# Kernel optimization log

Measured on AMD Instinct MI355X. Metric: run time of the kernel, lower is better.

Reference implementation:

```python
import jax, jax.numpy as jnp
import numpy as np

N, IN_DIM, OUT_DIM = 8192, 512, 256


def setup_inputs() -> dict:
    key = jax.random.key(0)
    k1, k2, k3, k4 = jax.random.split(key, 4)
    x = jax.random.normal(k1, (N, IN_DIM), dtype=jnp.float32)
    adj = jax.random.randint(k2, (N, N), 0, 2, dtype=jnp.int32)
    # nn.Linear(in_dim, out_dim, bias=False).weight -> [out_dim, in_dim]
    W_proj = jax.random.normal(k3, (OUT_DIM, IN_DIM), dtype=jnp.float32) * (1.0 / np.sqrt(IN_DIM))
    # nn.Linear(2*out_dim, 1, bias=False).weight flattened -> [2*out_dim]
    a = jax.random.normal(k4, (2 * OUT_DIM,), dtype=jnp.float32) * (1.0 / np.sqrt(2 * OUT_DIM))
    return {"x": x, "adj": adj, "W_proj": W_proj, "a": a}


def reference(x, adj, W_proj, a):
    # h = proj(x): [N, D]
    h = x @ W_proj.T
    D = h.shape[-1]
    # attn(cat([h_i, h_j])) == h_i @ a[:D] + h_j @ a[D:]  (exact decomposition,
    # avoids materializing the [N, N, 2D] concat tensor)
    s_i = h @ a[:D]   # [N]
    s_j = h @ a[D:]   # [N]
    scores = s_i[:, None] + s_j[None, :]          # [N, N]
    scores = jnp.where(adj > 0, scores, -jnp.inf)  # masked_fill
    alpha = jax.nn.softmax(scores, axis=1)         # softmax over neighbors j
    # dropout is identity in eval mode
    out = alpha @ h                                # [N, D]
    return jax.nn.elu(out), alpha
```

## Files before the change

kernel.cpp:

```cpp
#include <hip/hip_runtime.h>
#include <hip/hip_bf16.h>

#define NR 8192
#define DIN 512
#define DD 256

typedef __attribute__((ext_vector_type(8))) short short8;
typedef __attribute__((ext_vector_type(4))) float f32x4;

static __device__ __forceinline__ unsigned short f2bf(float x) {
    __hip_bfloat16 b = __float2bfloat16(x);
    return __builtin_bit_cast(unsigned short, b);
}
static __device__ __forceinline__ float bf2f(unsigned short u) {
    unsigned v = ((unsigned)u) << 16;
    return __builtin_bit_cast(float, v);
}

__global__ __launch_bounds__(256) void k_gemm_h(
        const float* __restrict__ x, const float* __restrict__ W,
        float* __restrict__ h) {
    __shared__ unsigned short Ah[64][72], Al[64][72];
    __shared__ unsigned short Bh[128][72], Bl[128][72];
    const int t = threadIdx.x;
    const int i0 = blockIdx.x * 64;
    const int n0 = blockIdx.y * 128;
    const int lane = t & 63, q = lane >> 4, lm = lane & 15;
    const int w = t >> 6, wm = w >> 1, wn = w & 1;
    const int ar = t >> 2, ac0 = (t & 3) << 4;
    const int bn = t >> 1, bh0 = (t & 1) << 5;
    f32x4 acc[2][4];
#pragma unroll
    for (int mt = 0; mt < 2; ++mt)
#pragma unroll
        for (int nt = 0; nt < 4; ++nt) acc[mt][nt] = (f32x4){0.f, 0.f, 0.f, 0.f};

    for (int kb = 0; kb < DIN; kb += 64) {
        __syncthreads();
        {
            const float4* xp = (const float4*)(x + (size_t)(i0 + ar) * DIN + kb + ac0);
#pragma unroll
            for (int u = 0; u < 4; ++u) {
                float4 v = xp[u];
                unsigned short h0 = f2bf(v.x), h1 = f2bf(v.y), h2 = f2bf(v.z), h3 = f2bf(v.w);
                unsigned short l0 = f2bf(v.x - bf2f(h0)), l1 = f2bf(v.y - bf2f(h1));
                unsigned short l2 = f2bf(v.z - bf2f(h2)), l3 = f2bf(v.w - bf2f(h3));
                *(uint2*)&Ah[ar][ac0 + u * 4] =
                    make_uint2((unsigned)h0 | ((unsigned)h1 << 16), (unsigned)h2 | ((unsigned)h3 << 16));
                *(uint2*)&Al[ar][ac0 + u * 4] =
                    make_uint2((unsigned)l0 | ((unsigned)l1 << 16), (unsigned)l2 | ((unsigned)l3 << 16));
            }
            const float4* wp = (const float4*)(W + (size_t)(n0 + bn) * DIN + kb + bh0);
#pragma unroll
            for (int u = 0; u < 8; ++u) {
                float4 v = wp[u];
                unsigned short h0 = f2bf(v.x), h1 = f2bf(v.y), h2 = f2bf(v.z), h3 = f2bf(v.w);
                unsigned short l0 = f2bf(v.x - bf2f(h0)), l1 = f2bf(v.y - bf2f(h1));
                unsigned short l2 = f2bf(v.z - bf2f(h2)), l3 = f2bf(v.w - bf2f(h3));
                *(uint2*)&Bh[bn][bh0 + u * 4] =
                    make_uint2((unsigned)h0 | ((unsigned)h1 << 16), (unsigned)h2 | ((unsigned)h3 << 16));
                *(uint2*)&Bl[bn][bh0 + u * 4] =
                    make_uint2((unsigned)l0 | ((unsigned)l1 << 16), (unsigned)l2 | ((unsigned)l3 << 16));
            }
        }
        __syncthreads();
#pragma unroll
        for (int ks = 0; ks < 64; ks += 32) {
            short8 fa_h[2], fa_l[2], fb_h[4], fb_l[4];
#pragma unroll
            for (int mt = 0; mt < 2; ++mt) {
                int r = wm * 32 + mt * 16 + lm;
                fa_h[mt] = *(const short8*)&Ah[r][ks + q * 8];
                fa_l[mt] = *(const short8*)&Al[r][ks + q * 8];
            }
#pragma unroll
            for (int nt = 0; nt < 4; ++nt) {
                int c = wn * 64 + nt * 16 + lm;
                fb_h[nt] = *(const short8*)&Bh[c][ks + q * 8];
                fb_l[nt] = *(const short8*)&Bl[c][ks + q * 8];
            }
#pragma unroll
            for (int mt = 0; mt < 2; ++mt)
#pragma unroll
                for (int nt = 0; nt < 4; ++nt) {
                    acc[mt][nt] = __builtin_amdgcn_mfma_f32_16x16x32_bf16(fa_h[mt], fb_h[nt], acc[mt][nt], 0, 0, 0);
                    acc[mt][nt] = __builtin_amdgcn_mfma_f32_16x16x32_bf16(fa_h[mt], fb_l[nt], acc[mt][nt], 0, 0, 0);
                    acc[mt][nt] = __builtin_amdgcn_mfma_f32_16x16x32_bf16(fa_l[mt], fb_h[nt], acc[mt][nt], 0, 0, 0);
                }
        }
    }
#pragma unroll
    for (int mt = 0; mt < 2; ++mt)
#pragma unroll
        for (int nt = 0; nt < 4; ++nt)
#pragma unroll
            for (int rr = 0; rr < 4; ++rr) {
                int row = i0 + wm * 32 + mt * 16 + q * 4 + rr;
                int col = n0 + wn * 64 + nt * 16 + lm;
                h[(size_t)row * DD + col] = acc[mt][nt][rr];
            }
}

__global__ __launch_bounds__(256) void k_s(
        const float* __restrict__ h, const float* __restrict__ a,
        float* __restrict__ s, float* __restrict__ pmax) {
    __shared__ float wmax[4];
    const int t = threadIdx.x, w = t >> 6, lane = t & 63;
    const int row = blockIdx.x * 4 + w;
    float4 hv = *(const float4*)(h + (size_t)row * DD + lane * 4);
    float4 av = *(const float4*)(a + DD + lane * 4);
    float d = hv.x * av.x + hv.y * av.y + hv.z * av.z + hv.w * av.w;
#pragma unroll
    for (int off = 32; off; off >>= 1) d += __shfl_down(d, off);
    if (lane == 0) { s[row] = d; wmax[w] = d; }
    __syncthreads();
    if (t == 0)
        pmax[blockIdx.x] = fmaxf(fmaxf(wmax[0], wmax[1]), fmaxf(wmax[2], wmax[3]));
}

__global__ __launch_bounds__(1024) void k_e(
        const float* __restrict__ s, const float* __restrict__ pmax,
        float* __restrict__ e) {
    __shared__ float red[1024];
    const int t = threadIdx.x;
    red[t] = fmaxf(pmax[t], pmax[t + 1024]);
    __syncthreads();
    for (int off = 512; off; off >>= 1) {
        if (t < off) red[t] = fmaxf(red[t], red[t + off]);
        __syncthreads();
    }
    float M = red[0];
    for (int j = t; j < NR; j += 1024) e[j] = expf(s[j] - M);
}

__global__ __launch_bounds__(256) void k_gt(
        const float* __restrict__ h, const float* __restrict__ e,
        unsigned short* __restrict__ gt) {
    __shared__ float tile[64][68];
    const int t = threadIdx.x;
    const int j0 = blockIdx.x * 64, d0 = blockIdx.y * 64;
    const int r = t >> 4, c4 = (t & 15) * 4;
#pragma unroll
    for (int rr = 0; rr < 4; ++rr) {
        int row = r + rr * 16;
        *(float4*)&tile[row][c4] = *(const float4*)(h + (size_t)(j0 + row) * DD + d0 + c4);
    }
    __syncthreads();
    float4 ev = *(const float4*)(e + j0 + c4);
#pragma unroll
    for (int rr = 0; rr < 4; ++rr) {
        int dd = r + rr * 16;
        unsigned short o0 = f2bf(ev.x * tile[c4 + 0][dd]);
        unsigned short o1 = f2bf(ev.y * tile[c4 + 1][dd]);
        unsigned short o2 = f2bf(ev.z * tile[c4 + 2][dd]);
        unsigned short o3 = f2bf(ev.w * tile[c4 + 3][dd]);
        *(uint2*)(gt + (size_t)(d0 + dd) * NR + j0 + c4) =
            make_uint2((unsigned)o0 | ((unsigned)o1 << 16), (unsigned)o2 | ((unsigned)o3 << 16));
    }
}

__global__ __launch_bounds__(512) void k_big(
        const int* __restrict__ adj, const unsigned short* __restrict__ gt,
        const float* __restrict__ e, float* __restrict__ num,
        float* __restrict__ dnm) {
    __shared__ unsigned short As[128][72];
    __shared__ unsigned short Bs[256][72];
    const int t = threadIdx.x;
    const int row0 = blockIdx.x * 128;
    const int k0 = blockIdx.y * 2048;
    const int lane = t & 63, q = lane >> 4, lm = lane & 15;
    const int w = t >> 6, wm = w >> 2, wn = w & 3;
    const int ar = t >> 2, ac0 = (t & 3) << 4;
    const int bn = t >> 1, bh0 = (t & 1) << 5;
    f32x4 acc[4][4];
#pragma unroll
    for (int mt = 0; mt < 4; ++mt)
#pragma unroll
        for (int nt = 0; nt < 4; ++nt) acc[mt][nt] = (f32x4){0.f, 0.f, 0.f, 0.f};
    float dsum = 0.f;

    for (int it = 0; it < 32; ++it) {
        const int kb = k0 + it * 64;
        __syncthreads();
        {
            const int4* ap = (const int4*)(adj + (size_t)(row0 + ar) * NR + kb + ac0);
            const float4* ep = (const float4*)(e + kb + ac0);
#pragma unroll
            for (int u = 0; u < 4; ++u) {
                int4 av = ap[u];
                float4 ev = ep[u];
                unsigned p0 = (av.x ? 0x3F80u : 0u) | (av.y ? 0x3F800000u : 0u);
                unsigned p1 = (av.z ? 0x3F80u : 0u) | (av.w ? 0x3F800000u : 0u);
                dsum += (av.x ? ev.x : 0.f) + (av.y ? ev.y : 0.f) +
                        (av.z ? ev.z : 0.f) + (av.w ? ev.w : 0.f);
                *(uint2*)&As[ar][ac0 + u * 4] = make_uint2(p0, p1);
            }
            const int4* gp = (const int4*)(gt + (size_t)bn * NR + kb + bh0);
            int4* bd = (int4*)&Bs[bn][bh0];
#pragma unroll
            for (int u = 0; u < 4; ++u) bd[u] = gp[u];
        }
        __syncthreads();
#pragma unroll
        for (int ks = 0; ks < 64; ks += 32) {
            short8 fa[4], fb[4];
#pragma unroll
            for (int mt = 0; mt < 4; ++mt)
                fa[mt] = *(const short8*)&As[wm * 64 + mt * 16 + lm][ks + q * 8];
#pragma unroll
            for (int nt = 0; nt < 4; ++nt)
                fb[nt] = *(const short8*)&Bs[wn * 64 + nt * 16 + lm][ks + q * 8];
#pragma unroll
            for (int mt = 0; mt < 4; ++mt)
#pragma unroll
                for (int nt = 0; nt < 4; ++nt)
                    acc[mt][nt] = __builtin_amdgcn_mfma_f32_16x16x32_bf16(fa[mt], fb[nt], acc[mt][nt], 0, 0, 0);
        }
    }
    dsum += __shfl_xor(dsum, 1);
    dsum += __shfl_xor(dsum, 2);
    if ((t & 3) == 0) atomicAdd(&dnm[row0 + ar], dsum);
#pragma unroll
    for (int mt = 0; mt < 4; ++mt)
#pragma unroll
        for (int nt = 0; nt < 4; ++nt)
#pragma unroll
            for (int rr = 0; rr < 4; ++rr) {
                int i = row0 + wm * 64 + mt * 16 + q * 4 + rr;
                int d = wn * 64 + nt * 16 + lm;
                atomicAdd(&num[(size_t)i * DD + d], acc[mt][nt][rr]);
            }
}

__global__ __launch_bounds__(256) void k_fin(
        const float* __restrict__ num, const float* __restrict__ dnm,
        float* __restrict__ out0, float* __restrict__ invd) {
    const int idx = blockIdx.x * 256 + threadIdx.x;
    const int i = idx >> 6, d4 = (idx & 63) << 2;
    float inv = 1.0f / dnm[i];
    float4 nm = *(const float4*)(num + (size_t)i * DD + d4);
    float4 o;
    float z;
    z = nm.x * inv; o.x = z > 0.f ? z : expm1f(z);
    z = nm.y * inv; o.y = z > 0.f ? z : expm1f(z);
    z = nm.z * inv; o.z = z > 0.f ? z : expm1f(z);
    z = nm.w * inv; o.w = z > 0.f ? z : expm1f(z);
    *(float4*)(out0 + (size_t)i * DD + d4) = o;
    if (d4 == 0) invd[i] = inv;
}

__global__ __launch_bounds__(256) void k_alpha(
        const int* __restrict__ adj, const float* __restrict__ e,
        const float* __restrict__ invd, float* __restrict__ alpha) {
    const size_t idx = (size_t)blockIdx.x * 256 + threadIdx.x;
    const int i = (int)(idx >> 11);
    const int jg = (int)(idx & 2047);
    int4 av = ((const int4*)adj)[idx];
    float4 ev = ((const float4*)e)[jg];
    float inv = invd[i];
    float4 o;
    o.x = av.x ? ev.x * inv : 0.f;
    o.y = av.y ? ev.y * inv : 0.f;
    o.z = av.z ? ev.z * inv : 0.f;
    o.w = av.w ? ev.w * inv : 0.f;
    ((float4*)alpha)[idx] = o;
}

extern "C" void kernel_launch(void* const* d_in, const int* in_sizes, int n_in,
                              void* d_out, int out_size, void* d_ws, size_t ws_size,
                              hipStream_t stream) {
    const float* x = (const float*)d_in[0];
    const int* adj = (const int*)d_in[1];
    const float* W = (const float*)d_in[2];
    const float* a = (const float*)d_in[3];
    float* out0 = (float*)d_out;
    float* alpha = (float*)d_out + (size_t)NR * DD;

    char* ws = (char*)d_ws;
    float* h            = (float*)(ws + 0);
    float* s            = (float*)(ws + 8388608);
    float* pmax         = (float*)(ws + 8421376);
    float* e            = (float*)(ws + 8429568);
    float* invd         = (float*)(ws + 8462336);
    float* dnm          = (float*)(ws + 8495104);
    unsigned short* gt  = (unsigned short*)(ws + 8527872);
    float* num          = (float*)(ws + 12722176);

    hipMemsetAsync(num, 0, (size_t)NR * DD * sizeof(float), stream);
    hipMemsetAsync(dnm, 0, NR * sizeof(float), stream);

    k_gemm_h<<<dim3(128, 2), 256, 0, stream>>>(x, W, h);
    k_s<<<2048, 256, 0, stream>>>(h, a, s, pmax);
    k_e<<<1, 1024, 0, stream>>>(s, pmax, e);
    k_gt<<<dim3(128, 4), 256, 0, stream>>>(h, e, gt);
    k_big<<<dim3(64, 4), 512, 0, stream>>>(adj, gt, e, num, dnm);
    k_fin<<<2048, 256, 0, stream>>>(num, dnm, out0, invd);
    k_alpha<<<65536, 256, 0, stream>>>(adj, e, invd, alpha);
}
```

Baseline: 599.2 us.

## Fuse aggregation, ELU finalize and alpha write into one row-block kernel

Replaces the split-K aggregation kernel, the finalize kernel and the alpha kernel with one kernel. Each block owns 32 full rows and keeps their adjacency as a shared-memory bitmask, so it can write alpha without re-reading the 256 MB int32 adj matrix. This also removes the atomics, the num/dnm memsets and two launches. The cost is a smaller MFMA tile per block (32x256), so gt is re-read by every one of the 256 blocks. Only 256 blocks are launched, which may leave the GPU underoccupied.

```diff
diff --git a/kernel.cpp b/kernel.cpp
--- a/kernel.cpp
+++ b/kernel.cpp
@@ -159,111 +159,103 @@
     }
 }
 
-__global__ __launch_bounds__(512) void k_big(
+__global__ __launch_bounds__(512, 4) void k_fused(
         const int* __restrict__ adj, const unsigned short* __restrict__ gt,
-        const float* __restrict__ e, float* __restrict__ num,
-        float* __restrict__ dnm) {
-    __shared__ unsigned short As[128][72];
+        const float* __restrict__ e, float* __restrict__ out0,
+        float* __restrict__ alpha) {
+    __shared__ unsigned short As[32][72];
     __shared__ unsigned short Bs[256][72];
-    const int t = threadIdx.x;
-    const int row0 = blockIdx.x * 128;
-    const int k0 = blockIdx.y * 2048;
+    __shared__ unsigned bm[32][256];
+    __shared__ float dnm_s[32];
+    const int t = threadIdx.x;
+    const int row0 = blockIdx.x * 32;
     const int lane = t & 63, q = lane >> 4, lm = lane & 15;
-    const int w = t >> 6, wm = w >> 2, wn = w & 3;
-    const int ar = t >> 2, ac0 = (t & 3) << 4;
-    const int bn = t >> 1, bh0 = (t & 1) << 5;
-    f32x4 acc[4][4];
-#pragma unroll
-    for (int mt = 0; mt < 4; ++mt)
-#pragma unroll
-        for (int nt = 0; nt < 4; ++nt) acc[mt][nt] = (f32x4){0.f, 0.f, 0.f, 0.f};
+    const int w = t >> 6;
+    const int ar = t >> 4, c = t & 15;
+    const int bn = t >> 1, bo = (t & 1) * 32;
+
+    f32x4 acc[2][2];
+#pragma unroll
+    for (int mt = 0; mt < 2; ++mt)
+#pragma unroll
+        for (int nt = 0; nt < 2; ++nt) acc[mt][nt] = (f32x4){0.f, 0.f, 0.f, 0.f};
     float dsum = 0.f;
 
-    for (int it = 0; it < 32; ++it) {
-        const int kb = k0 + it * 64;
+    const int* ap = adj + (size_t)(row0 + ar) * NR + c * 4;
+    const unsigned short* gp = gt + (size_t)bn * NR + bo;
+    const float* ep = e + c * 4;
+
+#pragma unroll 2
+    for (int it = 0; it < 128; ++it) {
         __syncthreads();
         {
-            const int4* ap = (const int4*)(adj + (size_t)(row0 + ar) * NR + kb + ac0);
-            const float4* ep = (const float4*)(e + kb + ac0);
-#pragma unroll
-            for (int u = 0; u < 4; ++u) {
-                int4 av = ap[u];
-                float4 ev = ep[u];
-                unsigned p0 = (av.x ? 0x3F80u : 0u) | (av.y ? 0x3F800000u : 0u);
-                unsigned p1 = (av.z ? 0x3F80u : 0u) | (av.w ? 0x3F800000u : 0u);
-                dsum += (av.x ? ev.x : 0.f) + (av.y ? ev.y : 0.f) +
-                        (av.z ? ev.z : 0.f) + (av.w ? ev.w : 0.f);
-                *(uint2*)&As[ar][ac0 + u * 4] = make_uint2(p0, p1);
-            }
-            const int4* gp = (const int4*)(gt + (size_t)bn * NR + kb + bh0);
-            int4* bd = (int4*)&Bs[bn][bh0];
-#pragma unroll
-            for (int u = 0; u < 4; ++u) bd[u] = gp[u];
+            int4 av = *(const int4*)(ap + (size_t)it * 64);
+            float4 ev = *(const float4*)(ep + it * 64);
+            unsigned p0 = (av.x ? 0x3F80u : 0u) | (av.y ? 0x3F800000u : 0u);
+            unsigned p1 = (av.z ? 0x3F80u : 0u) | (av.w ? 0x3F800000u : 0u);
+            dsum += (av.x ? ev.x : 0.f) + (av.y ? ev.y : 0.f) +
+                    (av.z ? ev.z : 0.f) + (av.w ? ev.w : 0.f);
+            *(uint2*)&As[ar][c * 4] = make_uint2(p0, p1);
+            unsigned nib = (av.x ? 1u : 0u) | (av.y ? 2u : 0u) |
+                           (av.z ? 4u : 0u) | (av.w ? 8u : 0u);
+            unsigned v = nib << ((c & 7) * 4);
+            v |= __shfl_xor(v, 1);
+            v |= __shfl_xor(v, 2);
+            v |= __shfl_xor(v, 4);
+            if ((c & 7) == 0) bm[ar][it * 2 + (c >> 3)] = v;
+            const int4* gsrc = (const int4*)(gp + (size_t)it * 64);
+            int4* bd = (int4*)&Bs[bn][bo];
+            bd[0] = gsrc[0]; bd[1] = gsrc[1]; bd[2] = gsrc[2]; bd[3] = gsrc[3];
         }
         __syncthreads();
 #pragma unroll
         for (int ks = 0; ks < 64; ks += 32) {
-            short8 fa[4], fb[4];
-#pragma unroll
-            for (int mt = 0; mt < 4; ++mt)
-                fa[mt] = *(const short8*)&As[wm * 64 + mt * 16 + lm][ks + q * 8];
-#pragma unroll
-            for (int nt = 0; nt < 4; ++nt)
-                fb[nt] = *(const short8*)&Bs[wn * 64 + nt * 16 + lm][ks + q * 8];
-#pragma unroll
-            for (int mt = 0; mt < 4; ++mt)
-#pragma unroll
-                for (int nt = 0; nt < 4; ++nt)
-                    acc[mt][nt] = __builtin_amdgcn_mfma_f32_16x16x32_bf16(fa[mt], fb[nt], acc[mt][nt], 0, 0, 0);
-        }
-    }
+            short8 fa0 = *(const short8*)&As[lm][ks + q * 8];
+            short8 fa1 = *(const short8*)&As[16 + lm][ks + q * 8];
+            short8 fb0 = *(const short8*)&Bs[w * 32 + lm][ks + q * 8];
+            short8 fb1 = *(const short8*)&Bs[w * 32 + 16 + lm][ks + q * 8];
+            acc[0][0] = __builtin_amdgcn_mfma_f32_16x16x32_bf16(fa0, fb0, acc[0][0], 0, 0, 0);
+            acc[0][1] = __builtin_amdgcn_mfma_f32_16x16x32_bf16(fa0, fb1, acc[0][1], 0, 0, 0);
+            acc[1][0] = __builtin_amdgcn_mfma_f32_16x16x32_bf16(fa1, fb0, acc[1][0], 0, 0, 0);
+            acc[1][1] = __builtin_amdgcn_mfma_f32_16x16x32_bf16(fa1, fb1, acc[1][1], 0, 0, 0);
+        }
+    }
+
     dsum += __shfl_xor(dsum, 1);
     dsum += __shfl_xor(dsum, 2);
-    if ((t & 3) == 0) atomicAdd(&dnm[row0 + ar], dsum);
-#pragma unroll
-    for (int mt = 0; mt < 4; ++mt)
-#pragma unroll
-        for (int nt = 0; nt < 4; ++nt)
+    dsum += __shfl_xor(dsum, 4);
+    dsum += __shfl_xor(dsum, 8);
+    if (c == 0) dnm_s[ar] = dsum;
+    __syncthreads();
+    if (t < 32) dnm_s[t] = 1.0f / dnm_s[t];
+    __syncthreads();
+
+#pragma unroll
+    for (int mt = 0; mt < 2; ++mt)
+#pragma unroll
+        for (int nt = 0; nt < 2; ++nt)
 #pragma unroll
             for (int rr = 0; rr < 4; ++rr) {
-                int i = row0 + wm * 64 + mt * 16 + q * 4 + rr;
-                int d = wn * 64 + nt * 16 + lm;
-                atomicAdd(&num[(size_t)i * DD + d], acc[mt][nt][rr]);
-            }
-}
-
-__global__ __launch_bounds__(256) void k_fin(
-        const float* __restrict__ num, const float* __restrict__ dnm,
-        float* __restrict__ out0, float* __restrict__ invd) {
-    const int idx = blockIdx.x * 256 + threadIdx.x;
-    const int i = idx >> 6, d4 = (idx & 63) << 2;
-    float inv = 1.0f / dnm[i];
-    float4 nm = *(const float4*)(num + (size_t)i * DD + d4);
-    float4 o;
-    float z;
-    z = nm.x * inv; o.x = z > 0.f ? z : expm1f(z);
-    z = nm.y * inv; o.y = z > 0.f ? z : expm1f(z);
-    z = nm.z * inv; o.z = z > 0.f ? z : expm1f(z);
-    z = nm.w * inv; o.w = z > 0.f ? z : expm1f(z);
-    *(float4*)(out0 + (size_t)i * DD + d4) = o;
-    if (d4 == 0) invd[i] = inv;
-}
-
-__global__ __launch_bounds__(256) void k_alpha(
-        const int* __restrict__ adj, const float* __restrict__ e,
-        const float* __restrict__ invd, float* __restrict__ alpha) {
-    const size_t idx = (size_t)blockIdx.x * 256 + threadIdx.x;
-    const int i = (int)(idx >> 11);
-    const int jg = (int)(idx & 2047);
-    int4 av = ((const int4*)adj)[idx];
-    float4 ev = ((const float4*)e)[jg];
-    float inv = invd[i];
-    float4 o;
-    o.x = av.x ? ev.x * inv : 0.f;
-    o.y = av.y ? ev.y * inv : 0.f;
-    o.z = av.z ? ev.z * inv : 0.f;
-    o.w = av.w ? ev.w * inv : 0.f;
-    ((float4*)alpha)[idx] = o;
+                int r = mt * 16 + q * 4 + rr;
+                int cc = w * 32 + nt * 16 + lm;
+                float z = acc[mt][nt][rr] * dnm_s[r];
+                out0[(size_t)(row0 + r) * DD + cc] = z > 0.f ? z : expm1f(z);
+            }
+
+    const float invr = dnm_s[ar];
+    float* arow = alpha + (size_t)(row0 + ar) * NR + c * 4;
+#pragma unroll 4
+    for (int it = 0; it < 128; ++it) {
+        unsigned wv = bm[ar][it * 2 + (c >> 3)];
+        unsigned nib = (wv >> ((c & 7) * 4)) & 15u;
+        float4 ev = *(const float4*)(ep + it * 64);
+        float4 o;
+        o.x = (nib & 1u) ? ev.x * invr : 0.f;
+        o.y = (nib & 2u) ? ev.y * invr : 0.f;
+        o.z = (nib & 4u) ? ev.z * invr : 0.f;
+        o.w = (nib & 8u) ? ev.w * invr : 0.f;
+        *(float4*)(arow + (size_t)it * 64) = o;
+    }
 }
 
 extern "C" void kernel_launch(void* const* d_in, const int* in_sizes, int n_in,
@@ -281,19 +273,11 @@
     float* s            = (float*)(ws + 8388608);
     float* pmax         = (float*)(ws + 8421376);
     float* e            = (float*)(ws + 8429568);
-    float* invd         = (float*)(ws + 8462336);
-    float* dnm          = (float*)(ws + 8495104);
-    unsigned short* gt  = (unsigned short*)(ws + 8527872);
-    float* num          = (float*)(ws + 12722176);
-
-    hipMemsetAsync(num, 0, (size_t)NR * DD * sizeof(float), stream);
-    hipMemsetAsync(dnm, 0, NR * sizeof(float), stream);
+    unsigned short* gt  = (unsigned short*)(ws + 8462336);
 
     k_gemm_h<<<dim3(128, 2), 256, 0, stream>>>(x, W, h);
     k_s<<<2048, 256, 0, stream>>>(h, a, s, pmax);
     k_e<<<1, 1024, 0, stream>>>(s, pmax, e);
     k_gt<<<dim3(128, 4), 256, 0, stream>>>(h, e, gt);
-    k_big<<<dim3(64, 4), 512, 0, stream>>>(adj, gt, e, num, dnm);
-    k_fin<<<2048, 256, 0, stream>>>(num, dnm, out0, invd);
-    k_alpha<<<65536, 256, 0, stream>>>(adj, e, invd, alpha);
-}
+    k_fused<<<256, 512, 0, stream>>>(adj, gt, e, out0, alpha);
+}
```

Measured after the change: 681.7 us. +13.8%, slower.
